# Performance work log

Measured on AMD Instinct MI355X. Metric: run time of the kernel, lower is better.

Reference implementation:

```python
import jax, jax.numpy as jnp
import numpy as np

B, S, H = 2, 2048, 4096          # batch, seq_len, hidden_size
NH, NKV, D = 32, 8, 128          # query heads, kv heads (GQA), head_dim
WINDOW = 1024                    # sliding window size
EPS = 1e-5
THETA = 10000.0


def setup_inputs() -> dict:
    key = jax.random.key(0)
    ks = jax.random.split(key, 5)
    w = lambda k, shape: jax.random.normal(k, shape, jnp.float32) * 0.02
    return {
        "hidden_states": jax.random.normal(ks[0], (B, S, H), jnp.float32),
        "wq": w(ks[1], (H, NH * D)),
        "wk": w(ks[2], (H, NKV * D)),
        "wv": w(ks[3], (H, NKV * D)),
        "wo": w(ks[4], (NH * D, H)),
        "q_norm_w": jnp.ones((D,), jnp.float32),
        "k_norm_w": jnp.ones((D,), jnp.float32),
    }


def _rmsnorm(x, w):
    # Exaone4RMSNorm over the last (head_dim) axis
    var = jnp.mean(jnp.square(x.astype(jnp.float32)), axis=-1, keepdims=True)
    return (x * jax.lax.rsqrt(var + EPS)).astype(x.dtype) * w


def _rotate_half(x):
    x1, x2 = jnp.split(x, 2, axis=-1)
    return jnp.concatenate([-x2, x1], axis=-1)


def reference(hidden_states, wq, wk, wv, wo, q_norm_w, k_norm_w):
    # QKV projections (no bias)
    q = (hidden_states @ wq).reshape(B, S, NH, D)
    k = (hidden_states @ wk).reshape(B, S, NKV, D)
    v = (hidden_states @ wv).reshape(B, S, NKV, D)
    # per-head QK RMSNorm, then [B, h, S, D] layout
    q = _rmsnorm(q, q_norm_w).transpose(0, 2, 1, 3)
    k = _rmsnorm(k, k_norm_w).transpose(0, 2, 1, 3)
    v = v.transpose(0, 2, 1, 3)
    # RoPE (applied on sliding-window layers in EXAONE4)
    pos = jnp.arange(S)
    inv_freq = 1.0 / (THETA ** (jnp.arange(0, D, 2, dtype=jnp.float32) / D))
    freqs = pos[:, None].astype(jnp.float32) * inv_freq[None, :]   # [S, D/2]
    emb = jnp.concatenate([freqs, freqs], axis=-1)                 # [S, D]
    cos, sin = jnp.cos(emb), jnp.sin(emb)
    q = q * cos + _rotate_half(q) * sin
    k = k * cos + _rotate_half(k) * sin
    # GQA: repeat kv heads to match query heads
    k = jnp.repeat(k, NH // NKV, axis=1)
    v = jnp.repeat(v, NH // NKV, axis=1)
    # SDPA with causal sliding-window mask: q_pos - WINDOW < k_pos <= q_pos
    scores = jnp.einsum('bhqd,bhkd->bhqk', q, k) / jnp.sqrt(jnp.float32(D))
    diff = pos[:, None] - pos[None, :]
    mask = (diff >= 0) & (diff < WINDOW)
    scores = jnp.where(mask, scores, jnp.finfo(scores.dtype).min)
    probs = jax.nn.softmax(scores, axis=-1)
    out = jnp.einsum('bhqk,bhkd->bhqd', probs, v)
    out = out.transpose(0, 2, 1, 3).reshape(B, S, NH * D)
    return out @ wo
```

## Files before the change

kernel.cpp:

```cpp
#include <hip/hip_runtime.h>
#include <hip/hip_bf16.h>

#define B_ 2
#define S_ 2048
#define H_ 4096
#define NH_ 32
#define NKV_ 8
#define D_ 128
#define WINDOW_ 1024
#define EPS_ 1e-5f
#define M_ (B_*S_)
#define NQKV_ ((NH_ + 2*NKV_) * D_)

typedef __attribute__((ext_vector_type(8))) __bf16 bf16x8;
typedef __attribute__((ext_vector_type(4))) float f32x4;
typedef __attribute__((ext_vector_type(16))) float f32x16;

__device__ __forceinline__ unsigned short f2bf(float f) {
  union { __hip_bfloat16 h; unsigned short us; } cv;
  cv.h = __float2bfloat16(f);
  return cv.us;
}
__device__ __forceinline__ float bf2f(unsigned short u) {
  union { __hip_bfloat16 h; unsigned short us; } cv;
  cv.us = u;
  return __bfloat162float(cv.h);
}

__device__ __forceinline__ void gload16(const unsigned short* g, unsigned short* l) {
  __builtin_amdgcn_global_load_lds(
      (const __attribute__((address_space(1))) unsigned int*)(const void*)g,
      (__attribute__((address_space(3))) unsigned int*)(void*)l, 16, 0, 0);
}

__global__ __launch_bounds__(256) void transpose_convert(
    const float* __restrict__ in, unsigned short* __restrict__ out, int K, int N) {
  __shared__ unsigned short t[64][72];
  const int n0 = blockIdx.x * 64, k0 = blockIdx.y * 64;
  const int tid = threadIdx.x;
  const int rr = tid >> 4, cc = (tid & 15) * 4;
  #pragma unroll
  for (int i = 0; i < 4; ++i) {
    const int r = i * 16 + rr;
    float4 v = *(const float4*)&in[(size_t)(k0 + r) * N + n0 + cc];
    t[cc + 0][r] = f2bf(v.x);
    t[cc + 1][r] = f2bf(v.y);
    t[cc + 2][r] = f2bf(v.z);
    t[cc + 3][r] = f2bf(v.w);
  }
  __syncthreads();
  #pragma unroll
  for (int i = 0; i < 4; ++i) {
    const int r = i * 16 + rr;
    ushort4 o;
    o.x = t[r][cc + 0]; o.y = t[r][cc + 1];
    o.z = t[r][cc + 2]; o.w = t[r][cc + 3];
    *(ushort4*)&out[(size_t)(n0 + r) * K + k0 + cc] = o;
  }
}

__global__ __launch_bounds__(256) void convert_bf16_kernel(
    const float* __restrict__ in, unsigned short* __restrict__ out, int n4) {
  int i = blockIdx.x * 256 + threadIdx.x;
  if (i >= n4) return;
  float4 v = ((const float4*)in)[i];
  ushort4 o;
  o.x = f2bf(v.x); o.y = f2bf(v.y); o.z = f2bf(v.z); o.w = f2bf(v.w);
  ((ushort4*)out)[i] = o;
}

template <bool OUT_BF16>
__global__ __launch_bounds__(512) void gemm12(
    const unsigned short* __restrict__ A, const unsigned short* __restrict__ Bt,
    void* __restrict__ Cout, int N, int K) {
  __shared__ __align__(16) unsigned short lds[2][28672];
  const int tid = threadIdx.x;
  const int wave = tid >> 6, lane = tid & 63;
  const int l15 = lane & 15, l16 = lane >> 4;
  const int m0 = blockIdx.y * 256, n0 = blockIdx.x * 192;
  const int wmi = wave >> 2, wni = wave & 3;

  const unsigned short* asrc[4];
  const unsigned short* bsrc[3];
  #pragma unroll
  for (int it = 0; it < 4; ++it) {
    const int d = it * 512 + tid;
    const int row = d >> 3, cis = (d & 7) ^ (row & 7);
    asrc[it] = A + (size_t)(m0 + row) * K + cis * 8;
  }
  #pragma unroll
  for (int it = 0; it < 3; ++it) {
    const int d = it * 512 + tid;
    const int row = d >> 3, cis = (d & 7) ^ (row & 7);
    bsrc[it] = Bt + (size_t)(n0 + row) * K + cis * 8;
  }

  int offA[2][8], offB[2][3];
  #pragma unroll
  for (int kk = 0; kk < 2; ++kk) {
    #pragma unroll
    for (int mi = 0; mi < 8; ++mi) {
      const int row = wmi * 128 + mi * 16 + l15;
      offA[kk][mi] = row * 64 + ((kk * 4 + l16) ^ (row & 7)) * 8;
    }
    #pragma unroll
    for (int ni = 0; ni < 3; ++ni) {
      const int row = wni * 48 + ni * 16 + l15;
      offB[kk][ni] = 16384 + row * 64 + ((kk * 4 + l16) ^ (row & 7)) * 8;
    }
  }

  f32x4 acc[8][3];
  #pragma unroll
  for (int mi = 0; mi < 8; ++mi)
    #pragma unroll
    for (int ni = 0; ni < 3; ++ni) acc[mi][ni] = (f32x4){0.f, 0.f, 0.f, 0.f};

#define PHASE_MFMA(MOFF)                                                     \
  asm volatile("s_waitcnt lgkmcnt(0)" ::: "memory");                         \
  __builtin_amdgcn_sched_barrier(0);                                         \
  __builtin_amdgcn_s_setprio(1);                                             \
  _Pragma("unroll") for (int i = 0; i < 4; ++i)                              \
    _Pragma("unroll") for (int j = 0; j < 3; ++j)                            \
      acc[(MOFF) + i][j] = __builtin_amdgcn_mfma_f32_16x16x32_bf16(          \
          av[i], bv[j], acc[(MOFF) + i][j], 0, 0, 0);                        \
  __builtin_amdgcn_s_setprio(0);                                             \
  __builtin_amdgcn_sched_barrier(0);

  #pragma unroll
  for (int it = 0; it < 4; ++it)
    gload16(asrc[it], &lds[0][it * 4096 + wave * 512]);
  #pragma unroll
  for (int it = 0; it < 3; ++it)
    gload16(bsrc[it], &lds[0][16384 + it * 4096 + wave * 512]);
  asm volatile("s_waitcnt vmcnt(0)" ::: "memory");
  __builtin_amdgcn_sched_barrier(0);
  __builtin_amdgcn_s_barrier();

  const int nk = K >> 6;
  for (int t = 0; t < nk; ++t) {
    const int cur = t & 1, nxt = cur ^ 1;
    const unsigned short* ldc = lds[cur];
    const bool dostg = (t + 1 < nk);
    const size_t ko = (size_t)(t + 1) * 64;
    bf16x8 av[4], bv[3];

    #pragma unroll
    for (int i = 0; i < 4; ++i) av[i] = *(const bf16x8*)&ldc[offA[0][i]];
    #pragma unroll
    for (int j = 0; j < 3; ++j) bv[j] = *(const bf16x8*)&ldc[offB[0][j]];
    if (dostg) {
      gload16(asrc[0] + ko, &lds[nxt][0 * 4096 + wave * 512]);
      gload16(asrc[1] + ko, &lds[nxt][1 * 4096 + wave * 512]);
    }
    __builtin_amdgcn_sched_barrier(0);
    __builtin_amdgcn_s_barrier();
    PHASE_MFMA(0)
    __builtin_amdgcn_s_barrier();

    #pragma unroll
    for (int i = 0; i < 4; ++i) av[i] = *(const bf16x8*)&ldc[offA[0][i + 4]];
    if (dostg) {
      gload16(asrc[2] + ko, &lds[nxt][2 * 4096 + wave * 512]);
      gload16(asrc[3] + ko, &lds[nxt][3 * 4096 + wave * 512]);
    }
    __builtin_amdgcn_sched_barrier(0);
    __builtin_amdgcn_s_barrier();
    PHASE_MFMA(4)
    __builtin_amdgcn_s_barrier();

    #pragma unroll
    for (int i = 0; i < 4; ++i) av[i] = *(const bf16x8*)&ldc[offA[1][i]];
    #pragma unroll
    for (int j = 0; j < 3; ++j) bv[j] = *(const bf16x8*)&ldc[offB[1][j]];
    if (dostg) {
      gload16(bsrc[0] + ko, &lds[nxt][16384 + 0 * 4096 + wave * 512]);
      gload16(bsrc[1] + ko, &lds[nxt][16384 + 1 * 4096 + wave * 512]);
    }
    __builtin_amdgcn_sched_barrier(0);
    __builtin_amdgcn_s_barrier();
    PHASE_MFMA(0)
    __builtin_amdgcn_s_barrier();

    #pragma unroll
    for (int i = 0; i < 4; ++i) av[i] = *(const bf16x8*)&ldc[offA[1][i + 4]];
    if (dostg) {
      gload16(bsrc[2] + ko, &lds[nxt][16384 + 2 * 4096 + wave * 512]);
    }
    __builtin_amdgcn_sched_barrier(0);
    __builtin_amdgcn_s_barrier();
    PHASE_MFMA(4)
    asm volatile("s_waitcnt vmcnt(0)" ::: "memory");
    __builtin_amdgcn_sched_barrier(0);
    __builtin_amdgcn_s_barrier();
  }
#undef PHASE_MFMA

  #pragma unroll
  for (int mi = 0; mi < 8; ++mi) {
    #pragma unroll
    for (int ni = 0; ni < 3; ++ni) {
      const int col = n0 + wni * 48 + ni * 16 + l15;
      #pragma unroll
      for (int j = 0; j < 4; ++j) {
        const int row = m0 + wmi * 128 + mi * 16 + l16 * 4 + j;
        if (OUT_BF16)
          ((unsigned short*)Cout)[(size_t)row * N + col] = f2bf(acc[mi][ni][j]);
        else
          ((float*)Cout)[(size_t)row * N + col] = acc[mi][ni][j];
      }
    }
  }
}

template <bool OUT_BF16>
__global__ __launch_bounds__(512) void gemm10(
    const unsigned short* __restrict__ A, const unsigned short* __restrict__ Bt,
    void* __restrict__ Cout, int N, int K) {
  __shared__ __align__(16) unsigned short lds[2][2][16384];
  const int tid = threadIdx.x;
  const int wave = tid >> 6, lane = tid & 63;
  const int l15 = lane & 15, l16 = lane >> 4;
  const int m0 = blockIdx.y * 256, n0 = blockIdx.x * 256;
  const int wmi = wave >> 2, wni = wave & 3;

  const unsigned short* asrc[4];
  const unsigned short* bsrc[4];
  #pragma unroll
  for (int it = 0; it < 4; ++it) {
    const int d = it * 512 + tid;
    const int row = d >> 3, cis = (d & 7) ^ (row & 7);
    asrc[it] = A + (size_t)(m0 + row) * K + cis * 8;
    bsrc[it] = Bt + (size_t)(n0 + row) * K + cis * 8;
  }

  int offA[2][8], offB[2][4];
  #pragma unroll
  for (int kk = 0; kk < 2; ++kk) {
    #pragma unroll
    for (int mi = 0; mi < 8; ++mi) {
      const int row = wmi * 128 + mi * 16 + l15;
      offA[kk][mi] = row * 64 + ((kk * 4 + l16) ^ (row & 7)) * 8;
    }
    #pragma unroll
    for (int ni = 0; ni < 4; ++ni) {
      const int row = wni * 64 + ni * 16 + l15;
      offB[kk][ni] = row * 64 + ((kk * 4 + l16) ^ (row & 7)) * 8;
    }
  }

  f32x4 acc[8][4];
  #pragma unroll
  for (int mi = 0; mi < 8; ++mi)
    #pragma unroll
    for (int ni = 0; ni < 4; ++ni) acc[mi][ni] = (f32x4){0.f, 0.f, 0.f, 0.f};

#define PHASE_MFMA(MOFF)                                                     \
  asm volatile("s_waitcnt lgkmcnt(0)" ::: "memory");                         \
  __builtin_amdgcn_sched_barrier(0);                                         \
  __builtin_amdgcn_s_setprio(1);                                             \
  _Pragma("unroll") for (int i = 0; i < 4; ++i)                              \
    _Pragma("unroll") for (int j = 0; j < 4; ++j)                            \
      acc[(MOFF) + i][j] = __builtin_amdgcn_mfma_f32_16x16x32_bf16(          \
          av[i], bv[j], acc[(MOFF) + i][j], 0, 0, 0);                        \
  __builtin_amdgcn_s_setprio(0);                                             \
  __builtin_amdgcn_sched_barrier(0);

  #pragma unroll
  for (int it = 0; it < 4; ++it) {
    gload16(asrc[it], &lds[0][0][it * 4096 + wave * 512]);
    gload16(bsrc[it], &lds[0][1][it * 4096 + wave * 512]);
  }
  asm volatile("s_waitcnt vmcnt(0)" ::: "memory");
  __builtin_amdgcn_sched_barrier(0);
  __builtin_amdgcn_s_barrier();

  const int nk = K >> 6;
  for (int t = 0; t < nk; ++t) {
    const int cur = t & 1, nxt = cur ^ 1;
    const unsigned short* as = lds[cur][0];
    const unsigned short* bs = lds[cur][1];
    const bool dostg = (t + 1 < nk);
    const size_t ko = (size_t)(t + 1) * 64;
    bf16x8 av[4], bv[4];

    #pragma unroll
    for (int i = 0; i < 4; ++i) av[i] = *(const bf16x8*)&as[offA[0][i]];
    #pragma unroll
    for (int j = 0; j < 4; ++j) bv[j] = *(const bf16x8*)&bs[offB[0][j]];
    if (dostg) {
      gload16(asrc[0] + ko, &lds[nxt][0][0 * 4096 + wave * 512]);
      gload16(asrc[1] + ko, &lds[nxt][0][1 * 4096 + wave * 512]);
    }
    __builtin_amdgcn_sched_barrier(0);
    __builtin_amdgcn_s_barrier();
    PHASE_MFMA(0)
    __builtin_amdgcn_s_barrier();

    #pragma unroll
    for (int i = 0; i < 4; ++i) av[i] = *(const bf16x8*)&as[offA[0][i + 4]];
    if (dostg) {
      gload16(asrc[2] + ko, &lds[nxt][0][2 * 4096 + wave * 512]);
      gload16(asrc[3] + ko, &lds[nxt][0][3 * 4096 + wave * 512]);
    }
    __builtin_amdgcn_sched_barrier(0);
    __builtin_amdgcn_s_barrier();
    PHASE_MFMA(4)
    __builtin_amdgcn_s_barrier();

    #pragma unroll
    for (int i = 0; i < 4; ++i) av[i] = *(const bf16x8*)&as[offA[1][i]];
    #pragma unroll
    for (int j = 0; j < 4; ++j) bv[j] = *(const bf16x8*)&bs[offB[1][j]];
    if (dostg) {
      gload16(bsrc[0] + ko, &lds[nxt][1][0 * 4096 + wave * 512]);
      gload16(bsrc[1] + ko, &lds[nxt][1][1 * 4096 + wave * 512]);
    }
    __builtin_amdgcn_sched_barrier(0);
    __builtin_amdgcn_s_barrier();
    PHASE_MFMA(0)
    __builtin_amdgcn_s_barrier();

    #pragma unroll
    for (int i = 0; i < 4; ++i) av[i] = *(const bf16x8*)&as[offA[1][i + 4]];
    if (dostg) {
      gload16(bsrc[2] + ko, &lds[nxt][1][2 * 4096 + wave * 512]);
      gload16(bsrc[3] + ko, &lds[nxt][1][3 * 4096 + wave * 512]);
    }
    __builtin_amdgcn_sched_barrier(0);
    __builtin_amdgcn_s_barrier();
    PHASE_MFMA(4)
    asm volatile("s_waitcnt vmcnt(0)" ::: "memory");
    __builtin_amdgcn_sched_barrier(0);
    __builtin_amdgcn_s_barrier();
  }
#undef PHASE_MFMA

  #pragma unroll
  for (int mi = 0; mi < 8; ++mi) {
    #pragma unroll
    for (int ni = 0; ni < 4; ++ni) {
      const int col = n0 + wni * 64 + ni * 16 + l15;
      #pragma unroll
      for (int j = 0; j < 4; ++j) {
        const int row = m0 + wmi * 128 + mi * 16 + l16 * 4 + j;
        if (OUT_BF16)
          ((unsigned short*)Cout)[(size_t)row * N + col] = f2bf(acc[mi][ni][j]);
        else
          ((float*)Cout)[(size_t)row * N + col] = acc[mi][ni][j];
      }
    }
  }
}

__global__ __launch_bounds__(256) void norm_rope_kernel(
    const unsigned short* __restrict__ QKVg,
    const float* __restrict__ qw, const float* __restrict__ kw,
    unsigned short* __restrict__ Qr, unsigned short* __restrict__ Kr) {
  const int bs = blockIdx.x;
  const int b = bs >> 11, s = bs & (S_ - 1);
  const int wave = threadIdx.x >> 6, lane = threadIdx.x & 63;

  float invf = 1.0f / powf(10000.0f, (float)lane * (1.0f / 64.0f));
  float sn, cs;
  sincosf((float)s * invf, &sn, &cs);

  const unsigned short* row = QKVg + (size_t)bs * NQKV_;
  const float qwa = qw[lane], qwb = qw[lane + 64];
  const float kwa = kw[lane], kwb = kw[lane + 64];
  const float scale = 0.08838834764831845f;

  for (int h = wave; h < NH_; h += 4) {
    float x0 = bf2f(row[h * D_ + lane]);
    float x1 = bf2f(row[h * D_ + 64 + lane]);
    float ss = x0 * x0 + x1 * x1;
    #pragma unroll
    for (int o = 32; o >= 1; o >>= 1) ss += __shfl_xor(ss, o);
    float r = rsqrtf(ss * (1.0f / 128.0f) + EPS_);
    x0 *= r * qwa; x1 *= r * qwb;
    float o0 = (x0 * cs - x1 * sn) * scale;
    float o1 = (x1 * cs + x0 * sn) * scale;
    size_t off = (((size_t)b * NH_ + h) * S_ + s) * D_;
    Qr[off + lane] = f2bf(o0);
    Qr[off + 64 + lane] = f2bf(o1);
  }
  for (int h = wave; h < NKV_; h += 4) {
    float x0 = bf2f(row[NH_ * D_ + h * D_ + lane]);
    float x1 = bf2f(row[NH_ * D_ + h * D_ + 64 + lane]);
    float ss = x0 * x0 + x1 * x1;
    #pragma unroll
    for (int o = 32; o >= 1; o >>= 1) ss += __shfl_xor(ss, o);
    float r = rsqrtf(ss * (1.0f / 128.0f) + EPS_);
    x0 *= r * kwa; x1 *= r * kwb;
    float o0 = x0 * cs - x1 * sn;
    float o1 = x1 * cs + x0 * sn;
    size_t off = (((size_t)b * NKV_ + h) * S_ + s) * D_;
    Kr[off + lane] = f2bf(o0);
    Kr[off + 64 + lane] = f2bf(o1);
  }
}

__global__ __launch_bounds__(256) void vtrans_kernel(
    const unsigned short* __restrict__ QKVg, unsigned short* __restrict__ Vt) {
  __shared__ unsigned short t[64][65];
  const int s0 = blockIdx.x * 64, d0 = blockIdx.y * 64;
  const int bh = blockIdx.z;
  const int b = bh >> 3, hk = bh & 7;
  const int tid = threadIdx.x;
  #pragma unroll
  for (int i = 0; i < 16; ++i) {
    int e = i * 256 + tid; int sr = e >> 6, dc = e & 63;
    t[sr][dc] = QKVg[(size_t)(b * S_ + s0 + sr) * NQKV_ + (NH_ + NKV_) * D_ + hk * D_ + d0 + dc];
  }
  __syncthreads();
  #pragma unroll
  for (int i = 0; i < 16; ++i) {
    int e = i * 256 + tid; int dr = e >> 6, sc = e & 63;
    Vt[((size_t)bh * D_ + d0 + dr) * S_ + s0 + sc] = t[sc][dr];
  }
}

__global__ __launch_bounds__(512) void attn_kernel(
    const unsigned short* __restrict__ Qr, const unsigned short* __restrict__ Kr,
    const unsigned short* __restrict__ Vt, unsigned short* __restrict__ Out) {
  const int q0 = blockIdx.x * 256;
  const int h = blockIdx.y, b = blockIdx.z, hk = h >> 2;
  const int tid = threadIdx.x;
  const int wave = tid >> 6, lane = tid & 63;
  const int l31 = lane & 31, hi = lane >> 5;
  const int qw0 = q0 + wave * 32;
  const int qpos = qw0 + l31;

  __shared__ __align__(16) unsigned short Ks[64 * 128];
  __shared__ __align__(16) unsigned short Vs[128 * 64];

  bf16x8 qf[8];
  {
    const unsigned short* qp = Qr + (((size_t)b * NH_ + h) * S_ + qpos) * D_ + hi * 8;
    #pragma unroll
    for (int ds = 0; ds < 8; ++ds) qf[ds] = *(const bf16x8*)(qp + ds * 16);
  }

  f32x16 o[4];
  #pragma unroll
  for (int i = 0; i < 4; ++i)
    #pragma unroll
    for (int j = 0; j < 16; ++j) o[i][j] = 0.f;
  float mrun = -1e30f, lrun = 0.f;

  const size_t kbase = ((size_t)b * NKV_ + hk) * S_;
  const size_t vbase = ((size_t)b * NKV_ + hk) * D_;

  const int ktlo = (q0 > 1023) ? ((q0 - 1023) & ~63) : 0;
  const int kthi = (q0 + 255) & ~63;
  const int wlo = (qw0 > 1023) ? ((qw0 - 1023) & ~63) : 0;
  const int whi = (qw0 + 31) & ~63;

  for (int kt = ktlo; kt <= kthi; kt += 64) {
    __syncthreads();
    #pragma unroll
    for (int it = 0; it < 2; ++it) {
      const int cb = it * 512 + wave * 64;
      const int c = cb + lane;
      const int rk = c >> 4, sk = c & 15;
      gload16(Kr + (kbase + kt + rk) * D_ + ((sk ^ (rk & 7)) * 8), Ks + (size_t)cb * 8);
      const int rv = c >> 3, sv = c & 7;
      gload16(Vt + (vbase + rv) * S_ + kt + ((sv ^ (rv & 7)) * 8), Vs + (size_t)cb * 8);
    }
    __syncthreads();
    if (kt < wlo || kt > whi) continue;

    f32x16 s0, s1;
    #pragma unroll
    for (int j = 0; j < 16; ++j) { s0[j] = 0.f; s1[j] = 0.f; }
    __builtin_amdgcn_s_setprio(1);
    #pragma unroll
    for (int ds = 0; ds < 8; ++ds) {
      const int g = ((ds * 2 + hi) ^ (l31 & 7)) * 8;
      bf16x8 k0 = *(const bf16x8*)&Ks[l31 * 128 + g];
      bf16x8 k1 = *(const bf16x8*)&Ks[(l31 + 32) * 128 + g];
      s0 = __builtin_amdgcn_mfma_f32_32x32x16_bf16(k0, qf[ds], s0, 0, 0, 0);
      s1 = __builtin_amdgcn_mfma_f32_32x32x16_bf16(k1, qf[ds], s1, 0, 0, 0);
    }
    __builtin_amdgcn_s_setprio(0);

    const bool fullValid = (kt + 63 <= qw0) && (kt >= qw0 - 992);
    if (!fullValid) {
      const int d0 = qpos - kt;
      #pragma unroll
      for (int r = 0; r < 16; ++r) {
        const int koff = (r & 3) + 8 * (r >> 2) + 4 * hi;
        if ((unsigned)(d0 - koff) >= (unsigned)WINDOW_) s0[r] = -1e30f;
        if ((unsigned)(d0 - koff - 32) >= (unsigned)WINDOW_) s1[r] = -1e30f;
      }
    }

    float pm = -1e30f;
    #pragma unroll
    for (int r = 0; r < 16; ++r) pm = fmaxf(pm, fmaxf(s0[r], s1[r]));
    pm = fmaxf(pm, __shfl_xor(pm, 32));
    if (!__all(pm - mrun <= 8.f)) {
      const float mnew = fmaxf(mrun, pm);
      const float scl = __expf(mrun - mnew);
      mrun = mnew;
      lrun *= scl;
      #pragma unroll
      for (int i = 0; i < 4; ++i)
        #pragma unroll
        for (int j = 0; j < 16; ++j) o[i][j] *= scl;
    }
    float ts = 0.f;
    #pragma unroll
    for (int r = 0; r < 16; ++r) {
      s0[r] = __expf(s0[r] - mrun); ts += s0[r];
      s1[r] = __expf(s1[r] - mrun); ts += s1[r];
    }
    ts += __shfl_xor(ts, 32);
    lrun += ts;

    unsigned pw[2][2][4];
    #pragma unroll
    for (int t2 = 0; t2 < 2; ++t2) {
      const f32x16 sv = t2 ? s1 : s0;
      #pragma unroll
      for (int sub = 0; sub < 2; ++sub) {
        const int bs4 = sub * 8;
        unsigned A0 = ((unsigned)f2bf(sv[bs4 + 1]) << 16) | f2bf(sv[bs4 + 0]);
        unsigned A1 = ((unsigned)f2bf(sv[bs4 + 3]) << 16) | f2bf(sv[bs4 + 2]);
        unsigned B0 = ((unsigned)f2bf(sv[bs4 + 5]) << 16) | f2bf(sv[bs4 + 4]);
        unsigned B1 = ((unsigned)f2bf(sv[bs4 + 7]) << 16) | f2bf(sv[bs4 + 6]);
        unsigned sA0 = __shfl_xor(A0, 32), sA1 = __shfl_xor(A1, 32);
        unsigned sB0 = __shfl_xor(B0, 32), sB1 = __shfl_xor(B1, 32);
        pw[t2][sub][0] = hi ? sB0 : A0;
        pw[t2][sub][1] = hi ? sB1 : A1;
        pw[t2][sub][2] = hi ? B0 : sA0;
        pw[t2][sub][3] = hi ? B1 : sA1;
      }
    }

    __builtin_amdgcn_s_setprio(1);
    #pragma unroll
    for (int t2 = 0; t2 < 2; ++t2)
      #pragma unroll
      for (int sub = 0; sub < 2; ++sub) {
        union { unsigned u[4]; bf16x8 v; } pb;
        pb.u[0] = pw[t2][sub][0]; pb.u[1] = pw[t2][sub][1];
        pb.u[2] = pw[t2][sub][2]; pb.u[3] = pw[t2][sub][3];
        #pragma unroll
        for (int dt = 0; dt < 4; ++dt) {
          const int rr = dt * 32 + l31;
          const int g = ((t2 * 4 + sub * 2 + hi) ^ (rr & 7)) * 8;
          bf16x8 vf = *(const bf16x8*)&Vs[rr * 64 + g];
          o[dt] = __builtin_amdgcn_mfma_f32_32x32x16_bf16(vf, pb.v, o[dt], 0, 0, 0);
        }
      }
    __builtin_amdgcn_s_setprio(0);
  }

  const float inv = 1.0f / lrun;
  unsigned short* op = Out + (size_t)(b * S_ + qpos) * (NH_ * D_) + h * D_;
  #pragma unroll
  for (int dt = 0; dt < 4; ++dt)
    #pragma unroll
    for (int g = 0; g < 4; ++g) {
      const int r = g * 4;
      uint2 val;
      val.x = ((unsigned)f2bf(o[dt][r + 1] * inv) << 16) | f2bf(o[dt][r + 0] * inv);
      val.y = ((unsigned)f2bf(o[dt][r + 3] * inv) << 16) | f2bf(o[dt][r + 2] * inv);
      *(uint2*)(op + dt * 32 + 8 * g + 4 * hi) = val;
    }
}

extern "C" void kernel_launch(void* const* d_in, const int* in_sizes, int n_in,
                              void* d_out, int out_size, void* d_ws, size_t ws_size,
                              hipStream_t stream) {
  const float* hidden = (const float*)d_in[0];
  const float* wq = (const float*)d_in[1];
  const float* wk = (const float*)d_in[2];
  const float* wv = (const float*)d_in[3];
  const float* wo = (const float*)d_in[4];
  const float* qw = (const float*)d_in[5];
  const float* kw = (const float*)d_in[6];
  float* out = (float*)d_out;

  char* ws = (char*)d_ws;
  unsigned short* wqkv = (unsigned short*)(ws);
  unsigned short* kr   = (unsigned short*)(ws);
  unsigned short* vt   = (unsigned short*)(ws + ((size_t)8 << 20));
  unsigned short* attn = (unsigned short*)(ws + ((size_t)16 << 20));
  unsigned short* qkvg = (unsigned short*)(ws + ((size_t)48 << 20));
  unsigned short* wot  = (unsigned short*)(ws + ((size_t)48 << 20));
  unsigned short* hb   = (unsigned short*)d_out;
  unsigned short* qr   = (unsigned short*)d_out + ((size_t)16 << 20);

  transpose_convert<<<dim3(NH_ * D_ / 64, H_ / 64), 256, 0, stream>>>(wq, wqkv, H_, NH_ * D_);
  transpose_convert<<<dim3(NKV_ * D_ / 64, H_ / 64), 256, 0, stream>>>(
      wk, wqkv + (size_t)NH_ * D_ * H_, H_, NKV_ * D_);
  transpose_convert<<<dim3(NKV_ * D_ / 64, H_ / 64), 256, 0, stream>>>(
      wv, wqkv + (size_t)(NH_ + NKV_) * D_ * H_, H_, NKV_ * D_);

  convert_bf16_kernel<<<(M_ * H_ / 4 + 255) / 256, 256, 0, stream>>>(hidden, hb, M_ * H_ / 4);

  gemm12<true><<<dim3(NQKV_ / 192, M_ / 256), 512, 0, stream>>>(hb, wqkv, qkvg, NQKV_, H_);

  norm_rope_kernel<<<M_, 256, 0, stream>>>(qkvg, qw, kw, qr, kr);

  vtrans_kernel<<<dim3(S_ / 64, D_ / 64, B_ * NKV_), 256, 0, stream>>>(qkvg, vt);

  transpose_convert<<<dim3(H_ / 64, H_ / 64), 256, 0, stream>>>(wo, wot, NH_ * D_, H_);

  attn_kernel<<<dim3(S_ / 256, NH_, B_), 512, 0, stream>>>(qr, kr, vt, attn);

  gemm10<false><<<dim3(H_ / 256, M_ / 256), 512, 0, stream>>>(attn, wot, out, H_, H_);
}
```

Before: 511.7 us.

## Shrink attention tiles, vectorize norm/rope and transpose stores, use exp2 softmax

Attention blocks shrink from 256 to 128 queries with 4 waves, which doubles the grid and cuts wasted key tiles at the window edges. The cost is more K/V loads per block. The norm/rope kernel now handles two heads per wave with paired bf16 loads and stores, and uses fast sincos/exp2 for the frequencies. It also folds log2(e) into the Q scale so softmax can use exp2. The transpose-convert kernel writes 16-byte vector stores from aligned LDS. Fast-math intrinsics may change numerics slightly.

```diff
diff --git a/kernel.cpp b/kernel.cpp
--- a/kernel.cpp
+++ b/kernel.cpp
@@ -35,7 +35,7 @@
 
 __global__ __launch_bounds__(256) void transpose_convert(
     const float* __restrict__ in, unsigned short* __restrict__ out, int K, int N) {
-  __shared__ unsigned short t[64][72];
+  __shared__ __align__(16) unsigned short t[64][72];
   const int n0 = blockIdx.x * 64, k0 = blockIdx.y * 64;
   const int tid = threadIdx.x;
   const int rr = tid >> 4, cc = (tid & 15) * 4;
@@ -50,12 +50,10 @@
   }
   __syncthreads();
   #pragma unroll
-  for (int i = 0; i < 4; ++i) {
-    const int r = i * 16 + rr;
-    ushort4 o;
-    o.x = t[r][cc + 0]; o.y = t[r][cc + 1];
-    o.z = t[r][cc + 2]; o.w = t[r][cc + 3];
-    *(ushort4*)&out[(size_t)(n0 + r) * K + k0 + cc] = o;
+  for (int i = 0; i < 2; ++i) {
+    const int s = i * 256 + tid;
+    const int n = s >> 3, kc = (s & 7) * 8;
+    *(uint4*)&out[(size_t)(n0 + n) * K + k0 + kc] = *(const uint4*)&t[n][kc];
   }
 }
 
@@ -360,43 +358,59 @@
   const int bs = blockIdx.x;
   const int b = bs >> 11, s = bs & (S_ - 1);
   const int wave = threadIdx.x >> 6, lane = threadIdx.x & 63;
-
-  float invf = 1.0f / powf(10000.0f, (float)lane * (1.0f / 64.0f));
-  float sn, cs;
-  sincosf((float)s * invf, &sn, &cs);
+  const int hi = lane >> 5, l31 = lane & 31;
+  const int p0 = 2 * l31;
+
+  const float c0 = -0.20762050593046015f;
+  float sn0, cs0, sn1, cs1;
+  __sincosf((float)s * exp2f(c0 * (float)p0), &sn0, &cs0);
+  __sincosf((float)s * exp2f(c0 * (float)(p0 + 1)), &sn1, &cs1);
 
   const unsigned short* row = QKVg + (size_t)bs * NQKV_;
-  const float qwa = qw[lane], qwb = qw[lane + 64];
-  const float kwa = kw[lane], kwb = kw[lane + 64];
-  const float scale = 0.08838834764831845f;
-
-  for (int h = wave; h < NH_; h += 4) {
-    float x0 = bf2f(row[h * D_ + lane]);
-    float x1 = bf2f(row[h * D_ + 64 + lane]);
-    float ss = x0 * x0 + x1 * x1;
-    #pragma unroll
-    for (int o = 32; o >= 1; o >>= 1) ss += __shfl_xor(ss, o);
-    float r = rsqrtf(ss * (1.0f / 128.0f) + EPS_);
-    x0 *= r * qwa; x1 *= r * qwb;
-    float o0 = (x0 * cs - x1 * sn) * scale;
-    float o1 = (x1 * cs + x0 * sn) * scale;
-    size_t off = (((size_t)b * NH_ + h) * S_ + s) * D_;
-    Qr[off + lane] = f2bf(o0);
-    Qr[off + 64 + lane] = f2bf(o1);
-  }
-  for (int h = wave; h < NKV_; h += 4) {
-    float x0 = bf2f(row[NH_ * D_ + h * D_ + lane]);
-    float x1 = bf2f(row[NH_ * D_ + h * D_ + 64 + lane]);
-    float ss = x0 * x0 + x1 * x1;
-    #pragma unroll
-    for (int o = 32; o >= 1; o >>= 1) ss += __shfl_xor(ss, o);
-    float r = rsqrtf(ss * (1.0f / 128.0f) + EPS_);
-    x0 *= r * kwa; x1 *= r * kwb;
-    float o0 = x0 * cs - x1 * sn;
-    float o1 = x1 * cs + x0 * sn;
-    size_t off = (((size_t)b * NKV_ + h) * S_ + s) * D_;
-    Kr[off + lane] = f2bf(o0);
-    Kr[off + 64 + lane] = f2bf(o1);
+  const float2 qwl = *(const float2*)&qw[p0];
+  const float2 qwh = *(const float2*)&qw[p0 + 64];
+  const float2 kwl = *(const float2*)&kw[p0];
+  const float2 kwh = *(const float2*)&kw[p0 + 64];
+  const float qscale = 0.08838834764831845f * 1.4426950408889634f;
+
+  #pragma unroll
+  for (int k = 0; k < 4; ++k) {
+    const int h = k * 8 + wave * 2 + hi;
+    const unsigned int xlo = *(const unsigned int*)&row[h * D_ + p0];
+    const unsigned int xhi = *(const unsigned int*)&row[h * D_ + 64 + p0];
+    float a0 = bf2f(xlo & 0xffff), a1 = bf2f(xlo >> 16);
+    float b0 = bf2f(xhi & 0xffff), b1 = bf2f(xhi >> 16);
+    float ss = a0 * a0 + a1 * a1 + b0 * b0 + b1 * b1;
+    #pragma unroll
+    for (int o = 16; o >= 1; o >>= 1) ss += __shfl_xor(ss, o);
+    const float r = rsqrtf(ss * (1.0f / 128.0f) + EPS_);
+    a0 *= r * qwl.x; a1 *= r * qwl.y; b0 *= r * qwh.x; b1 *= r * qwh.y;
+    const float o0 = (a0 * cs0 - b0 * sn0) * qscale;
+    const float o1 = (a1 * cs1 - b1 * sn1) * qscale;
+    const float o2 = (b0 * cs0 + a0 * sn0) * qscale;
+    const float o3 = (b1 * cs1 + a1 * sn1) * qscale;
+    const size_t off = (((size_t)b * NH_ + h) * S_ + s) * D_;
+    *(unsigned int*)&Qr[off + p0] = ((unsigned)f2bf(o1) << 16) | f2bf(o0);
+    *(unsigned int*)&Qr[off + 64 + p0] = ((unsigned)f2bf(o3) << 16) | f2bf(o2);
+  }
+  if (wave < 4) {
+    const int h = wave * 2 + hi;
+    const unsigned int xlo = *(const unsigned int*)&row[NH_ * D_ + h * D_ + p0];
+    const unsigned int xhi = *(const unsigned int*)&row[NH_ * D_ + h * D_ + 64 + p0];
+    float a0 = bf2f(xlo & 0xffff), a1 = bf2f(xlo >> 16);
+    float b0 = bf2f(xhi & 0xffff), b1 = bf2f(xhi >> 16);
+    float ss = a0 * a0 + a1 * a1 + b0 * b0 + b1 * b1;
+    #pragma unroll
+    for (int o = 16; o >= 1; o >>= 1) ss += __shfl_xor(ss, o);
+    const float r = rsqrtf(ss * (1.0f / 128.0f) + EPS_);
+    a0 *= r * kwl.x; a1 *= r * kwl.y; b0 *= r * kwh.x; b1 *= r * kwh.y;
+    const float o0 = a0 * cs0 - b0 * sn0;
+    const float o1 = a1 * cs1 - b1 * sn1;
+    const float o2 = b0 * cs0 + a0 * sn0;
+    const float o3 = b1 * cs1 + a1 * sn1;
+    const size_t off = (((size_t)b * NKV_ + h) * S_ + s) * D_;
+    *(unsigned int*)&Kr[off + p0] = ((unsigned)f2bf(o1) << 16) | f2bf(o0);
+    *(unsigned int*)&Kr[off + 64 + p0] = ((unsigned)f2bf(o3) << 16) | f2bf(o2);
   }
 }
 
@@ -420,10 +434,10 @@
   }
 }
 
-__global__ __launch_bounds__(512) void attn_kernel(
+__global__ __launch_bounds__(256) void attn_kernel(
     const unsigned short* __restrict__ Qr, const unsigned short* __restrict__ Kr,
     const unsigned short* __restrict__ Vt, unsigned short* __restrict__ Out) {
-  const int q0 = blockIdx.x * 256;
+  const int q0 = blockIdx.x * 128;
   const int h = blockIdx.y, b = blockIdx.z, hk = h >> 2;
   const int tid = threadIdx.x;
   const int wave = tid >> 6, lane = tid & 63;
@@ -452,18 +466,23 @@
   const size_t vbase = ((size_t)b * NKV_ + hk) * D_;
 
   const int ktlo = (q0 > 1023) ? ((q0 - 1023) & ~63) : 0;
-  const int kthi = (q0 + 255) & ~63;
+  const int kthi = (q0 + 127) & ~63;
   const int wlo = (qw0 > 1023) ? ((qw0 - 1023) & ~63) : 0;
   const int whi = (qw0 + 31) & ~63;
 
   for (int kt = ktlo; kt <= kthi; kt += 64) {
     __syncthreads();
     #pragma unroll
-    for (int it = 0; it < 2; ++it) {
-      const int cb = it * 512 + wave * 64;
+    for (int it = 0; it < 4; ++it) {
+      const int cb = it * 256 + wave * 64;
       const int c = cb + lane;
       const int rk = c >> 4, sk = c & 15;
       gload16(Kr + (kbase + kt + rk) * D_ + ((sk ^ (rk & 7)) * 8), Ks + (size_t)cb * 8);
+    }
+    #pragma unroll
+    for (int it = 0; it < 4; ++it) {
+      const int cb = it * 256 + wave * 64;
+      const int c = cb + lane;
       const int rv = c >> 3, sv = c & 7;
       gload16(Vt + (vbase + rv) * S_ + kt + ((sv ^ (rv & 7)) * 8), Vs + (size_t)cb * 8);
     }
@@ -501,7 +520,7 @@
     pm = fmaxf(pm, __shfl_xor(pm, 32));
     if (!__all(pm - mrun <= 8.f)) {
       const float mnew = fmaxf(mrun, pm);
-      const float scl = __expf(mrun - mnew);
+      const float scl = exp2f(mrun - mnew);
       mrun = mnew;
       lrun *= scl;
       #pragma unroll
@@ -509,12 +528,19 @@
         #pragma unroll
         for (int j = 0; j < 16; ++j) o[i][j] *= scl;
     }
-    float ts = 0.f;
-    #pragma unroll
-    for (int r = 0; r < 16; ++r) {
-      s0[r] = __expf(s0[r] - mrun); ts += s0[r];
-      s1[r] = __expf(s1[r] - mrun); ts += s1[r];
-    }
+    float tsA = 0.f, tsB = 0.f, tsC = 0.f, tsD = 0.f;
+    #pragma unroll
+    for (int r = 0; r < 16; r += 4) {
+      s0[r] = exp2f(s0[r] - mrun);     s1[r] = exp2f(s1[r] - mrun);
+      s0[r + 1] = exp2f(s0[r + 1] - mrun); s1[r + 1] = exp2f(s1[r + 1] - mrun);
+      s0[r + 2] = exp2f(s0[r + 2] - mrun); s1[r + 2] = exp2f(s1[r + 2] - mrun);
+      s0[r + 3] = exp2f(s0[r + 3] - mrun); s1[r + 3] = exp2f(s1[r + 3] - mrun);
+      tsA += s0[r] + s1[r];
+      tsB += s0[r + 1] + s1[r + 1];
+      tsC += s0[r + 2] + s1[r + 2];
+      tsD += s0[r + 3] + s1[r + 3];
+    }
+    float ts = (tsA + tsB) + (tsC + tsD);
     ts += __shfl_xor(ts, 32);
     lrun += ts;
 
@@ -609,7 +635,7 @@
 
   transpose_convert<<<dim3(H_ / 64, H_ / 64), 256, 0, stream>>>(wo, wot, NH_ * D_, H_);
 
-  attn_kernel<<<dim3(S_ / 256, NH_, B_), 512, 0, stream>>>(qr, kr, vt, attn);
+  attn_kernel<<<dim3(S_ / 128, NH_, B_), 256, 0, stream>>>(qr, kr, vt, attn);
 
   gemm10<false><<<dim3(H_ / 256, M_ / 256), 512, 0, stream>>>(attn, wot, out, H_, H_);
 }
```

New measurement: 579.1 us. 1.13x slower.
